# Kernel tuning notes

Hardware: AMD Instinct MI355X
Metric: run time of the kernel (lower is better)

Reference implementation:

```python
import jax, jax.numpy as jnp
import numpy as np
from jax import lax

T, N, E = 12, 10000, 160000
C_IN, C_H, C_OUT = 32, 64, 32
EPS = 1e-5


def _glorot(key, shape):
    fan_in, fan_out = shape[-2] if len(shape) > 1 else shape[0], shape[-1]
    s = (6.0 / (fan_in + fan_out)) ** 0.5
    return jax.random.uniform(key, shape, jnp.float32, -s, s)


def setup_inputs() -> dict:
    key = jax.random.key(0)
    ks = jax.random.split(key, 16)
    inp = {
        "x": jax.random.normal(ks[0], (T, N, C_IN), jnp.float32),
        "edge_index": jax.random.randint(ks[1], (2, E), 0, N, jnp.int32),
        "edge_weight": jax.random.uniform(ks[2], (E,), jnp.float32),
        # layer 1 (input layer): in=C_IN -> C_H
        "conv_w1": _glorot(ks[3], (C_H, C_IN, 3)) * 0.1,
        "conv_b1": jnp.zeros((C_H,), jnp.float32),
        "gamma1": jnp.ones((C_H,), jnp.float32),
        "beta1": jnp.zeros((C_H,), jnp.float32),
        "gcn_w1": _glorot(ks[4], (C_H, C_H)),
        "gcn_b1": jnp.zeros((C_H,), jnp.float32),
        # layer 2 (hidden layer): C_H -> C_H
        "conv_w2": _glorot(ks[5], (C_H, C_H, 3)) * 0.1,
        "conv_b2": jnp.zeros((C_H,), jnp.float32),
        "gamma2": jnp.ones((C_H,), jnp.float32),
        "beta2": jnp.zeros((C_H,), jnp.float32),
        "gcn_w2": _glorot(ks[6], (C_H, C_H)),
        "gcn_b2": jnp.zeros((C_H,), jnp.float32),
        # output linear: C_H -> C_OUT
        "out_w": _glorot(ks[7], (C_H, C_OUT)),
        "out_b": jnp.zeros((C_OUT,), jnp.float32),
    }
    return inp


def _stgcn_layer(x, edge_index, edge_weight, cw, cb, gamma, beta, gw, gb):
    # x: [T, N, C_in]  ->  torch.stack(x).permute(1,2,0) = [N, C_in, T]
    xs = jnp.transpose(x, (1, 2, 0))
    h = lax.conv_general_dilated(xs, cw, (1,), [(1, 1)],
                                 dimension_numbers=("NCH", "OIH", "NCH"))
    h = h + cb[None, :, None]
    # InstanceNorm1d(affine) over the temporal dim
    mu = h.mean(-1, keepdims=True)
    var = ((h - mu) ** 2).mean(-1, keepdims=True)
    h = (h - mu) * lax.rsqrt(var + EPS) * gamma[None, :, None] + beta[None, :, None]
    h = jax.nn.relu(h)
    h = jnp.transpose(h, (2, 0, 1))  # [T, N, C_out]
    # GCNConv per timestep (vectorized over T)
    src, dst = edge_index[0], edge_index[1]
    n = h.shape[1]
    deg = jnp.zeros((n,), h.dtype).at[dst].add(edge_weight) + 1.0  # self-loop weight 1
    dis = lax.rsqrt(deg)
    norm = dis[src] * edge_weight * dis[dst]  # [E]
    xw = jnp.einsum("tnc,cd->tnd", h, gw)  # [T, N, C_out]
    msg = xw[:, src, :] * norm[None, :, None]  # [T, E, C_out]
    agg = jax.vmap(lambda m: jax.ops.segment_sum(m, dst, num_segments=n))(msg)
    agg = agg + (dis * dis)[None, :, None] * xw + gb  # self loop + bias
    return agg


def reference(x, edge_index, edge_weight,
              conv_w1, conv_b1, gamma1, beta1, gcn_w1, gcn_b1,
              conv_w2, conv_b2, gamma2, beta2, gcn_w2, gcn_b2,
              out_w, out_b):
    h = _stgcn_layer(x, edge_index, edge_weight,
                     conv_w1, conv_b1, gamma1, beta1, gcn_w1, gcn_b1)
    h = _stgcn_layer(h, edge_index, edge_weight,
                     conv_w2, conv_b2, gamma2, beta2, gcn_w2, gcn_b2)
    out = jnp.einsum("tnc,co->tno", h, out_w) + out_b  # per-t linear
    return out.mean(axis=0)  # [N, C_OUT]
```

## Files before the change

kernel.cpp:

```cpp
#include <hip/hip_runtime.h>
#include <hip/hip_bf16.h>
#include <stdint.h>

#define MAXDEG 64

typedef short s16x8 __attribute__((ext_vector_type(8)));
typedef short s16x4 __attribute__((ext_vector_type(4)));
typedef float f32x4 __attribute__((ext_vector_type(4)));

static __device__ __forceinline__ float us2f(unsigned short u) {
    union { float f; unsigned int i; } cv; cv.i = ((unsigned int)u) << 16; return cv.f;
}
static __device__ __forceinline__ unsigned short f2us(float f) {
    __hip_bfloat16 h = __float2bfloat16(f);
    return *(unsigned short*)&h;
}

#define WIMG_TOTAL 30720

__global__ void k_build_ell(const int* __restrict__ ei, const float* __restrict__ ew,
                            float* __restrict__ deg, unsigned* __restrict__ cnt,
                            int2* __restrict__ ell, int E)
{
    int e = blockIdx.x * 256 + threadIdx.x;
    if (e >= E) return;
    int s = ei[e], d = ei[E + e];
    float w = ew[e];
    atomicAdd(&deg[d], w);
    unsigned slot = atomicAdd(&cnt[d], 1u);
    if (slot < MAXDEG) ell[(size_t)d * MAXDEG + slot] = make_int2(s, __float_as_int(w));
}

__global__ void k_norm(int2* __restrict__ ell, const unsigned* __restrict__ cnt,
                       const float* __restrict__ deg, int N)
{
    int idx = blockIdx.x * 256 + threadIdx.x;
    if (idx >= N * MAXDEG) return;
    int n = idx >> 6;
    int s = idx & (MAXDEG - 1);
    unsigned dg = cnt[n]; if (dg > MAXDEG) dg = MAXDEG;
    if ((unsigned)s >= dg) return;
    int2 p = ell[idx];
    unsigned sx = (unsigned)p.x;
    float nrm = (sx < (unsigned)N)
        ? rsqrtf(deg[sx] + 1.0f) * __int_as_float(p.y) * rsqrtf(deg[n] + 1.0f) : 0.f;
    ell[idx] = make_int2(p.x, __float_as_int(nrm));
}

__global__ void k_prep(const float* __restrict__ cw1, const float* __restrict__ gw1,
                       const float* __restrict__ cw2, const float* __restrict__ gw2,
                       unsigned short* __restrict__ wimg)
{
    int idx = blockIdx.x * 256 + threadIdx.x;
    if (idx >= WIMG_TOTAL) return;
    float v = 0.f;
    if (idx < 7680) {
        int kk = idx / 2560, r = idx - kk * 2560, cc = r / 40, ci = r - cc * 40;
        if (ci < 32) v = cw1[(cc * 32 + ci) * 3 + kk];
    } else if (idx < 12288) {
        int j = idx - 7680, d = j / 72, cc = j - d * 72;
        if (cc < 64) v = gw1[cc * 64 + d];
    } else if (idx < 26112) {
        int j = idx - 12288;
        int kk = j / 4608, r = j - kk * 4608, cc = r / 72, ci = r - cc * 72;
        if (ci < 64) v = cw2[(cc * 64 + ci) * 3 + kk];
    } else {
        int j = idx - 26112, d = j / 72, cc = j - d * 72;
        if (cc < 64) v = gw2[cc * 64 + d];
    }
    wimg[idx] = f2us(v);
}

#define ACCE(NRM, V0, V1, V2)                                                          \
    a[0] = fmaf(NRM, us2f(V0.x), a[0]);  a[1] = fmaf(NRM, us2f(V0.y), a[1]);           \
    a[2] = fmaf(NRM, us2f(V0.z), a[2]);  a[3] = fmaf(NRM, us2f(V0.w), a[3]);           \
    a[4] = fmaf(NRM, us2f(V1.x), a[4]);  a[5] = fmaf(NRM, us2f(V1.y), a[5]);           \
    a[6] = fmaf(NRM, us2f(V1.z), a[6]);  a[7] = fmaf(NRM, us2f(V1.w), a[7]);           \
    a[8] = fmaf(NRM, us2f(V2.x), a[8]);  a[9] = fmaf(NRM, us2f(V2.y), a[9]);           \
    a[10] = fmaf(NRM, us2f(V2.z), a[10]); a[11] = fmaf(NRM, us2f(V2.w), a[11]);

template<int CIN>
__global__ __launch_bounds__(1024, 4) void k_layer_a(
    const float* __restrict__ x_in,
    const unsigned short* __restrict__ wimg,
    const float* __restrict__ gm, const float* __restrict__ bt,
    unsigned short* __restrict__ xw_out, int N)
{
    constexpr int KT   = CIN / 32;
    constexpr int WSTR = (CIN == 64) ? 72 : 40;
    __shared__ __align__(16) short WT[3 * 64 * WSTR];
    __shared__ __align__(16) short gwT[64 * 72];
    __shared__ __align__(16) short xh[16][14 * 72];

    const int tid = threadIdx.x;
    const int nn = tid >> 6;
    const int c = tid & 63;
    const int m = c & 15;
    const int q = c >> 4;
    const int mrow = (m < 12) ? m : 11;
    int n = blockIdx.x * 16 + nn;
    if (n >= N) n = N - 1;

    {
        const uint4* wt1  = (const uint4*)(wimg);
        const uint4* gwt1 = (const uint4*)(wimg + 7680);
        if (tid < 960) ((uint4*)WT)[tid]  = wt1[tid];
        if (tid < 576) ((uint4*)gwT)[tid] = gwt1[tid];
    }
    #pragma unroll
    for (int it = 0; it < (12 * CIN) / 128; ++it) {
        int i2 = it * 128 + c * 2;
        int t = i2 / CIN, ci = i2 - t * CIN;
        float2 xv = *(const float2*)&x_in[((size_t)t * N + n) * CIN + ci];
        xh[nn][(t + 1) * 72 + ci]     = (short)f2us(xv.x);
        xh[nn][(t + 1) * 72 + ci + 1] = (short)f2us(xv.y);
    }
    if (c < CIN) { xh[nn][c] = 0; xh[nn][13 * 72 + c] = 0; }
    __syncthreads();

    f32x4 acc[4];
    #pragma unroll
    for (int nt = 0; nt < 4; ++nt) acc[nt] = (f32x4){0.f, 0.f, 0.f, 0.f};
    #pragma unroll
    for (int kk = 0; kk < 3; ++kk) {
        #pragma unroll
        for (int kt = 0; kt < KT; ++kt) {
            s16x8 aA = *(const s16x8*)&xh[nn][(mrow + kk) * 72 + kt * 32 + q * 8];
            #pragma unroll
            for (int nt = 0; nt < 4; ++nt) {
                s16x8 bB = *(const s16x8*)&WT[kk * (64 * WSTR) + (nt * 16 + m) * WSTR + kt * 32 + q * 8];
                acc[nt] = __builtin_amdgcn_mfma_f32_16x16x32_bf16(aA, bB, acc[nt], 0, 0, 0);
            }
        }
    }

    #pragma unroll
    for (int nt = 0; nt < 4; ++nt) {
        float s  = acc[nt][0] + acc[nt][1] + acc[nt][2] + acc[nt][3];
        float s2 = acc[nt][0] * acc[nt][0] + acc[nt][1] * acc[nt][1]
                 + acc[nt][2] * acc[nt][2] + acc[nt][3] * acc[nt][3];
        if (q == 3) { s = 0.f; s2 = 0.f; }
        s  += __shfl_xor(s, 16);  s  += __shfl_xor(s, 32);
        s2 += __shfl_xor(s2, 16); s2 += __shfl_xor(s2, 32);
        const float mu  = s * (1.f / 12.f);
        const float var = s2 * (1.f / 12.f) - mu * mu;
        const float scn = rsqrtf(var + 1e-5f) * gm[nt * 16 + m];
        const float sbn = bt[nt * 16 + m];
        if (q < 3) {
            #pragma unroll
            for (int reg = 0; reg < 4; ++reg) {
                float hv = fmaf(acc[nt][reg] - mu, scn, sbn);
                hv = hv > 0.f ? hv : 0.f;
                xh[nn][(q * 4 + reg) * 72 + nt * 16 + m] = (short)f2us(hv);
            }
        }
    }

    s16x8 a2[2];
    #pragma unroll
    for (int kt2 = 0; kt2 < 2; ++kt2)
        a2[kt2] = *(const s16x8*)&xh[nn][mrow * 72 + kt2 * 32 + q * 8];
    f32x4 acc2[4];
    #pragma unroll
    for (int nt = 0; nt < 4; ++nt) acc2[nt] = (f32x4){0.f, 0.f, 0.f, 0.f};
    #pragma unroll
    for (int nt = 0; nt < 4; ++nt) {
        #pragma unroll
        for (int kt2 = 0; kt2 < 2; ++kt2) {
            s16x8 b2 = *(const s16x8*)&gwT[(nt * 16 + m) * 72 + kt2 * 32 + q * 8];
            acc2[nt] = __builtin_amdgcn_mfma_f32_16x16x32_bf16(a2[kt2], b2, acc2[nt], 0, 0, 0);
        }
    }

    unsigned short* dst = xw_out + (size_t)n * 768;
    if (q < 3) {
        #pragma unroll
        for (int nt = 0; nt < 4; ++nt)
            #pragma unroll
            for (int reg = 0; reg < 4; ++reg)
                dst[(q * 4 + reg) * 64 + nt * 16 + m] = f2us(acc2[nt][reg]);
    }
}

__global__ __launch_bounds__(512, 4) void k_gather_a(
    const unsigned short* __restrict__ xw_in,
    const int2* __restrict__ ell, const unsigned* __restrict__ cnt,
    const float* __restrict__ deg, const float* __restrict__ gb,
    const unsigned short* __restrict__ wimg,
    const float* __restrict__ gm, const float* __restrict__ bt,
    unsigned short* __restrict__ rowmean, int N)
{
    constexpr int WSTR = 72;
    __shared__ __align__(16) short WT[3 * 64 * WSTR];
    __shared__ __align__(16) short gwT[64 * 72];
    __shared__ __align__(16) short xh[8][14 * 72];

    const int tid = threadIdx.x;
    const int nn = tid >> 6;
    const int L = tid & 63;
    const int m = L & 15;
    const int q = L >> 4;
    const int mrow = (m < 12) ? m : 11;
    int n = blockIdx.x * 8 + nn;
    if (n >= N) n = N - 1;

    const int2* row = ell + (size_t)n * MAXDEG;
    int2 pl = row[L];
    unsigned dg = cnt[n]; if (dg > MAXDEG) dg = MAXDEG;
    const float dn = rsqrtf(deg[n] + 1.0f);
    const float d2 = dn * dn;
    const unsigned short* self = xw_in + (size_t)n * 768 + L * 4;
    ushort4 v0 = *(const ushort4*)self;
    ushort4 v1 = *(const ushort4*)(self + 256);
    ushort4 v2 = *(const ushort4*)(self + 512);

    {
        const uint4* wt2  = (const uint4*)(wimg + 12288);
        const uint4* gwt2 = (const uint4*)(wimg + 26112);
        for (int g = tid; g < 1728; g += 512) ((uint4*)WT)[g]  = wt2[g];
        for (int g = tid; g < 576;  g += 512) ((uint4*)gwT)[g] = gwt2[g];
    }
    xh[nn][L] = 0; xh[nn][13 * 72 + L] = 0;
    __syncthreads();

    float a[12];
    {
        const int c0 = (L * 4) & 63;
        const float g0 = gb[c0], g1 = gb[c0 + 1], g2 = gb[c0 + 2], g3 = gb[c0 + 3];
        a[0] = fmaf(d2, us2f(v0.x), g0); a[1] = fmaf(d2, us2f(v0.y), g1);
        a[2] = fmaf(d2, us2f(v0.z), g2); a[3] = fmaf(d2, us2f(v0.w), g3);
        a[4] = fmaf(d2, us2f(v1.x), g0); a[5] = fmaf(d2, us2f(v1.y), g1);
        a[6] = fmaf(d2, us2f(v1.z), g2); a[7] = fmaf(d2, us2f(v1.w), g3);
        a[8] = fmaf(d2, us2f(v2.x), g0); a[9] = fmaf(d2, us2f(v2.y), g1);
        a[10] = fmaf(d2, us2f(v2.z), g2); a[11] = fmaf(d2, us2f(v2.w), g3);
    }

    unsigned e = 0;
    for (; e + 8 <= dg; e += 8) {
        ushort4 B0[8], B1[8], B2[8];
        float NR[8];
        #pragma unroll
        for (int i = 0; i < 8; ++i) {
            unsigned sx = (unsigned)__builtin_amdgcn_readlane(pl.x, (int)(e + i));
            NR[i] = __int_as_float(__builtin_amdgcn_readlane(pl.y, (int)(e + i)));
            if (sx >= (unsigned)N) sx = 0;
            const unsigned short* qp = xw_in + (size_t)sx * 768 + L * 4;
            B0[i] = *(const ushort4*)qp;
            B1[i] = *(const ushort4*)(qp + 256);
            B2[i] = *(const ushort4*)(qp + 512);
        }
        #pragma unroll
        for (int i = 0; i < 8; ++i) { ACCE(NR[i], B0[i], B1[i], B2[i]) }
    }
    if (e + 4 <= dg) {
        ushort4 B0[4], B1[4], B2[4];
        float NR[4];
        #pragma unroll
        for (int i = 0; i < 4; ++i) {
            unsigned sx = (unsigned)__builtin_amdgcn_readlane(pl.x, (int)(e + i));
            NR[i] = __int_as_float(__builtin_amdgcn_readlane(pl.y, (int)(e + i)));
            if (sx >= (unsigned)N) sx = 0;
            const unsigned short* qp = xw_in + (size_t)sx * 768 + L * 4;
            B0[i] = *(const ushort4*)qp;
            B1[i] = *(const ushort4*)(qp + 256);
            B2[i] = *(const ushort4*)(qp + 512);
        }
        #pragma unroll
        for (int i = 0; i < 4; ++i) { ACCE(NR[i], B0[i], B1[i], B2[i]) }
        e += 4;
    }
    for (; e < dg; ++e) {
        unsigned sx = (unsigned)__builtin_amdgcn_readlane(pl.x, (int)e);
        float nr = __int_as_float(__builtin_amdgcn_readlane(pl.y, (int)e));
        if (sx >= (unsigned)N) sx = 0;
        const unsigned short* qp = xw_in + (size_t)sx * 768 + L * 4;
        ushort4 w0 = *(const ushort4*)qp;
        ushort4 w1 = *(const ushort4*)(qp + 256);
        ushort4 w2 = *(const ushort4*)(qp + 512);
        ACCE(nr, w0, w1, w2)
    }

    #pragma unroll
    for (int j = 0; j < 3; ++j) {
        s16x4 s4 = { (short)f2us(a[j * 4 + 0]), (short)f2us(a[j * 4 + 1]),
                     (short)f2us(a[j * 4 + 2]), (short)f2us(a[j * 4 + 3]) };
        *(s16x4*)&xh[nn][(j * 4 + q + 1) * 72 + ((L * 4) & 63)] = s4;
    }

    f32x4 acc[4];
    #pragma unroll
    for (int nt = 0; nt < 4; ++nt) acc[nt] = (f32x4){0.f, 0.f, 0.f, 0.f};
    #pragma unroll
    for (int kk = 0; kk < 3; ++kk) {
        #pragma unroll
        for (int kt = 0; kt < 2; ++kt) {
            s16x8 aA = *(const s16x8*)&xh[nn][(mrow + kk) * 72 + kt * 32 + q * 8];
            #pragma unroll
            for (int nt = 0; nt < 4; ++nt) {
                s16x8 bB = *(const s16x8*)&WT[kk * (64 * WSTR) + (nt * 16 + m) * WSTR + kt * 32 + q * 8];
                acc[nt] = __builtin_amdgcn_mfma_f32_16x16x32_bf16(aA, bB, acc[nt], 0, 0, 0);
            }
        }
    }

    #pragma unroll
    for (int nt = 0; nt < 4; ++nt) {
        float s  = acc[nt][0] + acc[nt][1] + acc[nt][2] + acc[nt][3];
        float s2 = acc[nt][0] * acc[nt][0] + acc[nt][1] * acc[nt][1]
                 + acc[nt][2] * acc[nt][2] + acc[nt][3] * acc[nt][3];
        if (q == 3) { s = 0.f; s2 = 0.f; }
        s  += __shfl_xor(s, 16);  s  += __shfl_xor(s, 32);
        s2 += __shfl_xor(s2, 16); s2 += __shfl_xor(s2, 32);
        const float mu  = s * (1.f / 12.f);
        const float var = s2 * (1.f / 12.f) - mu * mu;
        const float scn = rsqrtf(var + 1e-5f) * gm[nt * 16 + m];
        const float sbn = bt[nt * 16 + m];
        if (q < 3) {
            #pragma unroll
            for (int reg = 0; reg < 4; ++reg) {
                float hv = fmaf(acc[nt][reg] - mu, scn, sbn);
                hv = hv > 0.f ? hv : 0.f;
                xh[nn][(q * 4 + reg) * 72 + nt * 16 + m] = (short)f2us(hv);
            }
        }
    }

    s16x8 a2[2];
    #pragma unroll
    for (int kt2 = 0; kt2 < 2; ++kt2)
        a2[kt2] = *(const s16x8*)&xh[nn][mrow * 72 + kt2 * 32 + q * 8];
    f32x4 acc2[4];
    #pragma unroll
    for (int nt = 0; nt < 4; ++nt) acc2[nt] = (f32x4){0.f, 0.f, 0.f, 0.f};
    #pragma unroll
    for (int nt = 0; nt < 4; ++nt) {
        #pragma unroll
        for (int kt2 = 0; kt2 < 2; ++kt2) {
            s16x8 b2 = *(const s16x8*)&gwT[(nt * 16 + m) * 72 + kt2 * 32 + q * 8];
            acc2[nt] = __builtin_amdgcn_mfma_f32_16x16x32_bf16(a2[kt2], b2, acc2[nt], 0, 0, 0);
        }
    }

    #pragma unroll
    for (int nt = 0; nt < 4; ++nt) {
        float pm = (q < 3) ? (acc2[nt][0] + acc2[nt][1] + acc2[nt][2] + acc2[nt][3]) : 0.f;
        pm += __shfl_xor(pm, 16); pm += __shfl_xor(pm, 32);
        if (q == 0)
            rowmean[(size_t)n * 64 + nt * 16 + m] = f2us(pm * (1.f / 12.f));
    }
}

#define FIN_E(EIDX)                                                                    \
    {                                                                                  \
        unsigned sx = (unsigned)__builtin_amdgcn_readlane(pl.x, (int)(EIDX));          \
        float nrm = __int_as_float(__builtin_amdgcn_readlane(pl.y, (int)(EIDX)));      \
        if (sx >= (unsigned)N) sx = 0;                                                 \
        a = fmaf(nrm, us2f(rowmean[(size_t)sx * 64 + L]), a);                          \
    }

__global__ __launch_bounds__(256) void k_final(
    const unsigned short* __restrict__ rowmean, const int2* __restrict__ ell,
    const unsigned* __restrict__ cnt, const float* __restrict__ deg,
    const float* __restrict__ gb,
    const float* __restrict__ ow, const float* __restrict__ ob,
    float* __restrict__ dout, int N)
{
    __shared__ __align__(16) float hbuf[4][64];
    const int tid = threadIdx.x;
    const int nn = tid >> 6, L = tid & 63;
    int n = blockIdx.x * 4 + nn;
    if (n >= N) n = N - 1;
    const float dn = rsqrtf(deg[n] + 1.0f);
    const float d2 = dn * dn;

    const int2* row = ell + (size_t)n * MAXDEG;
    int2 pl = row[L];
    unsigned dg = cnt[n]; if (dg > MAXDEG) dg = MAXDEG;

    float a = fmaf(d2, us2f(rowmean[(size_t)n * 64 + L]), gb[L]);

    unsigned e = 0;
    for (; e + 7 < dg; e += 8) {
        FIN_E(e)     FIN_E(e + 1) FIN_E(e + 2) FIN_E(e + 3)
        FIN_E(e + 4) FIN_E(e + 5) FIN_E(e + 6) FIN_E(e + 7)
    }
    for (; e < dg; ++e) { FIN_E(e) }

    hbuf[nn][L] = a;
    __syncthreads();
    if (L < 32) {
        float oa = ob[L];
        #pragma unroll
        for (int cc = 0; cc < 64; ++cc)
            oa = fmaf(hbuf[nn][cc], ow[cc * 32 + L], oa);
        dout[(size_t)n * 32 + L] = oa;
    }
}

extern "C" void kernel_launch(void* const* d_in, const int* in_sizes, int n_in,
                              void* d_out, int out_size, void* d_ws, size_t ws_size,
                              hipStream_t stream)
{
    const float* x   = (const float*)d_in[0];
    const int*   ei  = (const int*)d_in[1];
    const float* ew  = (const float*)d_in[2];
    const float* cw1 = (const float*)d_in[3];
    const float* gm1 = (const float*)d_in[5];
    const float* bt1 = (const float*)d_in[6];
    const float* gw1 = (const float*)d_in[7];
    const float* gb1 = (const float*)d_in[8];
    const float* cw2 = (const float*)d_in[9];
    const float* gm2 = (const float*)d_in[11];
    const float* bt2 = (const float*)d_in[12];
    const float* gw2 = (const float*)d_in[13];
    const float* gb2 = (const float*)d_in[14];
    const float* ow  = (const float*)d_in[15];
    const float* ob  = (const float*)d_in[16];

    const int N = in_sizes[0] / (12 * 32);
    const int E = in_sizes[2];

    char* p0 = (char*)d_ws;
    char* p = p0;
    float* deg = (float*)p;          p += (size_t)N * 4;
    unsigned* cnt = (unsigned*)p;    p += (size_t)N * 4;
    p = (char*)(((uintptr_t)p + 255) & ~(uintptr_t)255);
    int2* ell = (int2*)p;            p += (size_t)N * MAXDEG * 8;
    p = (char*)(((uintptr_t)p + 255) & ~(uintptr_t)255);
    unsigned short* wimg = (unsigned short*)p; p += (size_t)WIMG_TOTAL * 2;
    p = (char*)(((uintptr_t)p + 255) & ~(uintptr_t)255);
    unsigned short* bufXW1 = (unsigned short*)p; p += (size_t)N * 768 * 2;
    unsigned short* rowmean = (unsigned short*)p; p += (size_t)N * 64 * 2;

    const size_t need = (size_t)(p - p0);
    if (ws_size < need) {
        hipMemsetAsync(d_out, 0, (size_t)out_size * 4, stream);
        return;
    }

    hipMemsetAsync(deg, 0, (size_t)N * 8, stream);

    const int eb   = (E + 255) / 256;
    const int nb16 = (N + 15) / 16;
    const int nb8  = (N + 7) / 8;
    const int nb4  = (N + 3) / 4;
    k_prep<<<(WIMG_TOTAL + 255) / 256, 256, 0, stream>>>(cw1, gw1, cw2, gw2, wimg);
    k_build_ell<<<eb, 256, 0, stream>>>(ei, ew, deg, cnt, ell, E);
    k_norm<<<(N * MAXDEG + 255) / 256, 256, 0, stream>>>(ell, cnt, deg, N);

    k_layer_a<32><<<nb16, 1024, 0, stream>>>(x, wimg, gm1, bt1, bufXW1, N);
    k_gather_a<<<nb8, 512, 0, stream>>>(bufXW1, ell, cnt, deg, gb1,
                                        wimg, gm2, bt2, rowmean, N);
    k_final<<<nb4, 256, 0, stream>>>(rowmean, ell, cnt, deg, gb2, ow, ob, (float*)d_out, N);
}
```

Baseline: 177.9 us.

## Fuse ELL build into layer-1 kernel, compute edge norm on the fly, widen gathers

The separate ELL-build and normalization kernels are removed. Edge insertion now runs in extra blocks appended to the layer-1 conv/GCN launch, and the per-edge normalization is recomputed inside the gather and final kernels from deg[src]. Gathers of the bf16 XW rows use one 16-byte load plus one 8-byte load per neighbor instead of three 8-byte loads, with the channel mapping and the shared-memory writes changed to match. This saves two launches and a pass over the ELL array, at the cost of an extra deg[] lookup and rsqrt per edge and mixing atomic-heavy blocks with MFMA blocks in one grid.

After: 169.6 us. 1.05x faster.

```diff
diff --git a/kernel.cpp b/kernel.cpp
--- a/kernel.cpp
+++ b/kernel.cpp
@@ -17,35 +17,6 @@
 }
 
 #define WIMG_TOTAL 30720
-
-__global__ void k_build_ell(const int* __restrict__ ei, const float* __restrict__ ew,
-                            float* __restrict__ deg, unsigned* __restrict__ cnt,
-                            int2* __restrict__ ell, int E)
-{
-    int e = blockIdx.x * 256 + threadIdx.x;
-    if (e >= E) return;
-    int s = ei[e], d = ei[E + e];
-    float w = ew[e];
-    atomicAdd(&deg[d], w);
-    unsigned slot = atomicAdd(&cnt[d], 1u);
-    if (slot < MAXDEG) ell[(size_t)d * MAXDEG + slot] = make_int2(s, __float_as_int(w));
-}
-
-__global__ void k_norm(int2* __restrict__ ell, const unsigned* __restrict__ cnt,
-                       const float* __restrict__ deg, int N)
-{
-    int idx = blockIdx.x * 256 + threadIdx.x;
-    if (idx >= N * MAXDEG) return;
-    int n = idx >> 6;
-    int s = idx & (MAXDEG - 1);
-    unsigned dg = cnt[n]; if (dg > MAXDEG) dg = MAXDEG;
-    if ((unsigned)s >= dg) return;
-    int2 p = ell[idx];
-    unsigned sx = (unsigned)p.x;
-    float nrm = (sx < (unsigned)N)
-        ? rsqrtf(deg[sx] + 1.0f) * __int_as_float(p.y) * rsqrtf(deg[n] + 1.0f) : 0.f;
-    ell[idx] = make_int2(p.x, __float_as_int(nrm));
-}
 
 __global__ void k_prep(const float* __restrict__ cw1, const float* __restrict__ gw1,
                        const float* __restrict__ cw2, const float* __restrict__ gw2,
@@ -71,21 +42,39 @@
     wimg[idx] = f2us(v);
 }
 
-#define ACCE(NRM, V0, V1, V2)                                                          \
-    a[0] = fmaf(NRM, us2f(V0.x), a[0]);  a[1] = fmaf(NRM, us2f(V0.y), a[1]);           \
-    a[2] = fmaf(NRM, us2f(V0.z), a[2]);  a[3] = fmaf(NRM, us2f(V0.w), a[3]);           \
-    a[4] = fmaf(NRM, us2f(V1.x), a[4]);  a[5] = fmaf(NRM, us2f(V1.y), a[5]);           \
-    a[6] = fmaf(NRM, us2f(V1.z), a[6]);  a[7] = fmaf(NRM, us2f(V1.w), a[7]);           \
-    a[8] = fmaf(NRM, us2f(V2.x), a[8]);  a[9] = fmaf(NRM, us2f(V2.y), a[9]);           \
-    a[10] = fmaf(NRM, us2f(V2.z), a[10]); a[11] = fmaf(NRM, us2f(V2.w), a[11]);
+#define BLO(u) __uint_as_float((unsigned)(u) << 16)
+#define BHI(u) __uint_as_float((unsigned)(u) & 0xffff0000u)
+
+#define ACC2(NRM, WA, WB)                                                              \
+    a[0] = fmaf(NRM, BLO(WA.x), a[0]);   a[1] = fmaf(NRM, BHI(WA.x), a[1]);            \
+    a[2] = fmaf(NRM, BLO(WA.y), a[2]);   a[3] = fmaf(NRM, BHI(WA.y), a[3]);            \
+    a[4] = fmaf(NRM, BLO(WA.z), a[4]);   a[5] = fmaf(NRM, BHI(WA.z), a[5]);            \
+    a[6] = fmaf(NRM, BLO(WA.w), a[6]);   a[7] = fmaf(NRM, BHI(WA.w), a[7]);            \
+    a[8] = fmaf(NRM, us2f(WB.x), a[8]);  a[9] = fmaf(NRM, us2f(WB.y), a[9]);           \
+    a[10] = fmaf(NRM, us2f(WB.z), a[10]); a[11] = fmaf(NRM, us2f(WB.w), a[11]);
 
 template<int CIN>
-__global__ __launch_bounds__(1024, 4) void k_layer_a(
+__global__ __launch_bounds__(1024, 4) void k_layer_build(
     const float* __restrict__ x_in,
     const unsigned short* __restrict__ wimg,
     const float* __restrict__ gm, const float* __restrict__ bt,
-    unsigned short* __restrict__ xw_out, int N)
+    unsigned short* __restrict__ xw_out, int N, int NB,
+    const int* __restrict__ ei, const float* __restrict__ ew,
+    float* __restrict__ deg, unsigned* __restrict__ cnt,
+    int2* __restrict__ ell, int E)
 {
+    if ((int)blockIdx.x >= NB) {
+        int e = ((int)blockIdx.x - NB) * 1024 + (int)threadIdx.x;
+        if (e < E) {
+            int s = ei[e], d = ei[E + e];
+            float w = ew[e];
+            atomicAdd(&deg[d], w);
+            unsigned slot = atomicAdd(&cnt[d], 1u);
+            if (slot < MAXDEG) ell[(size_t)d * MAXDEG + slot] = make_int2(s, __float_as_int(w));
+        }
+        return;
+    }
+
     constexpr int KT   = CIN / 32;
     constexpr int WSTR = (CIN == 64) ? 72 : 40;
     __shared__ __align__(16) short WT[3 * 64 * WSTR];
@@ -209,10 +198,9 @@
     unsigned dg = cnt[n]; if (dg > MAXDEG) dg = MAXDEG;
     const float dn = rsqrtf(deg[n] + 1.0f);
     const float d2 = dn * dn;
-    const unsigned short* self = xw_in + (size_t)n * 768 + L * 4;
-    ushort4 v0 = *(const ushort4*)self;
-    ushort4 v1 = *(const ushort4*)(self + 256);
-    ushort4 v2 = *(const ushort4*)(self + 512);
+    const unsigned short* sp = xw_in + (size_t)n * 768;
+    uint4   sA = *(const uint4*)(sp + 8 * L);
+    ushort4 sB = *(const ushort4*)(sp + 512 + 4 * L);
 
     {
         const uint4* wt2  = (const uint4*)(wimg + 12288);
@@ -225,66 +213,68 @@
 
     float a[12];
     {
-        const int c0 = (L * 4) & 63;
-        const float g0 = gb[c0], g1 = gb[c0 + 1], g2 = gb[c0 + 2], g3 = gb[c0 + 3];
-        a[0] = fmaf(d2, us2f(v0.x), g0); a[1] = fmaf(d2, us2f(v0.y), g1);
-        a[2] = fmaf(d2, us2f(v0.z), g2); a[3] = fmaf(d2, us2f(v0.w), g3);
-        a[4] = fmaf(d2, us2f(v1.x), g0); a[5] = fmaf(d2, us2f(v1.y), g1);
-        a[6] = fmaf(d2, us2f(v1.z), g2); a[7] = fmaf(d2, us2f(v1.w), g3);
-        a[8] = fmaf(d2, us2f(v2.x), g0); a[9] = fmaf(d2, us2f(v2.y), g1);
-        a[10] = fmaf(d2, us2f(v2.z), g2); a[11] = fmaf(d2, us2f(v2.w), g3);
+        const int cb1 = 8 * (L & 7);
+        const int cb2 = (4 * L) & 63;
+        a[0] = fmaf(d2, BLO(sA.x), gb[cb1 + 0]); a[1] = fmaf(d2, BHI(sA.x), gb[cb1 + 1]);
+        a[2] = fmaf(d2, BLO(sA.y), gb[cb1 + 2]); a[3] = fmaf(d2, BHI(sA.y), gb[cb1 + 3]);
+        a[4] = fmaf(d2, BLO(sA.z), gb[cb1 + 4]); a[5] = fmaf(d2, BHI(sA.z), gb[cb1 + 5]);
+        a[6] = fmaf(d2, BLO(sA.w), gb[cb1 + 6]); a[7] = fmaf(d2, BHI(sA.w), gb[cb1 + 7]);
+        a[8] = fmaf(d2, us2f(sB.x), gb[cb2 + 0]); a[9]  = fmaf(d2, us2f(sB.y), gb[cb2 + 1]);
+        a[10] = fmaf(d2, us2f(sB.z), gb[cb2 + 2]); a[11] = fmaf(d2, us2f(sB.w), gb[cb2 + 3]);
     }
 
     unsigned e = 0;
     for (; e + 8 <= dg; e += 8) {
-        ushort4 B0[8], B1[8], B2[8];
-        float NR[8];
+        uint4 A[8]; ushort4 Bv[8]; float NR[8];
         #pragma unroll
         for (int i = 0; i < 8; ++i) {
-            unsigned sx = (unsigned)__builtin_amdgcn_readlane(pl.x, (int)(e + i));
-            NR[i] = __int_as_float(__builtin_amdgcn_readlane(pl.y, (int)(e + i)));
-            if (sx >= (unsigned)N) sx = 0;
-            const unsigned short* qp = xw_in + (size_t)sx * 768 + L * 4;
-            B0[i] = *(const ushort4*)qp;
-            B1[i] = *(const ushort4*)(qp + 256);
-            B2[i] = *(const ushort4*)(qp + 512);
-        }
-        #pragma unroll
-        for (int i = 0; i < 8; ++i) { ACCE(NR[i], B0[i], B1[i], B2[i]) }
+            unsigned sxr = (unsigned)__builtin_amdgcn_readlane(pl.x, (int)(e + i));
+            float w = __int_as_float(__builtin_amdgcn_readlane(pl.y, (int)(e + i)));
+            unsigned sx = (sxr < (unsigned)N) ? sxr : 0u;
+            float nr = rsqrtf(deg[sx] + 1.0f) * w * dn;
+            NR[i] = (sxr < (unsigned)N) ? nr : 0.f;
+            const unsigned short* qp = xw_in + (size_t)sx * 768;
+            A[i]  = *(const uint4*)(qp + 8 * L);
+            Bv[i] = *(const ushort4*)(qp + 512 + 4 * L);
+        }
+        #pragma unroll
+        for (int i = 0; i < 8; ++i) { ACC2(NR[i], A[i], Bv[i]) }
     }
     if (e + 4 <= dg) {
-        ushort4 B0[4], B1[4], B2[4];
-        float NR[4];
+        uint4 A[4]; ushort4 Bv[4]; float NR[4];
         #pragma unroll
         for (int i = 0; i < 4; ++i) {
-            unsigned sx = (unsigned)__builtin_amdgcn_readlane(pl.x, (int)(e + i));
-            NR[i] = __int_as_float(__builtin_amdgcn_readlane(pl.y, (int)(e + i)));
-            if (sx >= (unsigned)N) sx = 0;
-            const unsigned short* qp = xw_in + (size_t)sx * 768 + L * 4;
-            B0[i] = *(const ushort4*)qp;
-            B1[i] = *(const ushort4*)(qp + 256);
-            B2[i] = *(const ushort4*)(qp + 512);
-        }
-        #pragma unroll
-        for (int i = 0; i < 4; ++i) { ACCE(NR[i], B0[i], B1[i], B2[i]) }
+            unsigned sxr = (unsigned)__builtin_amdgcn_readlane(pl.x, (int)(e + i));
+            float w = __int_as_float(__builtin_amdgcn_readlane(pl.y, (int)(e + i)));
+            unsigned sx = (sxr < (unsigned)N) ? sxr : 0u;
+            float nr = rsqrtf(deg[sx] + 1.0f) * w * dn;
+            NR[i] = (sxr < (unsigned)N) ? nr : 0.f;
+            const unsigned short* qp = xw_in + (size_t)sx * 768;
+            A[i]  = *(const uint4*)(qp + 8 * L);
+            Bv[i] = *(const ushort4*)(qp + 512 + 4 * L);
+        }
+        #pragma unroll
+        for (int i = 0; i < 4; ++i) { ACC2(NR[i], A[i], Bv[i]) }
         e += 4;
     }
     for (; e < dg; ++e) {
-        unsigned sx = (unsigned)__builtin_amdgcn_readlane(pl.x, (int)e);
-        float nr = __int_as_float(__builtin_amdgcn_readlane(pl.y, (int)e));
-        if (sx >= (unsigned)N) sx = 0;
-        const unsigned short* qp = xw_in + (size_t)sx * 768 + L * 4;
-        ushort4 w0 = *(const ushort4*)qp;
-        ushort4 w1 = *(const ushort4*)(qp + 256);
-        ushort4 w2 = *(const ushort4*)(qp + 512);
-        ACCE(nr, w0, w1, w2)
-    }
-
-    #pragma unroll
-    for (int j = 0; j < 3; ++j) {
-        s16x4 s4 = { (short)f2us(a[j * 4 + 0]), (short)f2us(a[j * 4 + 1]),
-                     (short)f2us(a[j * 4 + 2]), (short)f2us(a[j * 4 + 3]) };
-        *(s16x4*)&xh[nn][(j * 4 + q + 1) * 72 + ((L * 4) & 63)] = s4;
+        unsigned sxr = (unsigned)__builtin_amdgcn_readlane(pl.x, (int)e);
+        float w = __int_as_float(__builtin_amdgcn_readlane(pl.y, (int)e));
+        unsigned sx = (sxr < (unsigned)N) ? sxr : 0u;
+        float nr = rsqrtf(deg[sx] + 1.0f) * w * dn;
+        if (sxr >= (unsigned)N) nr = 0.f;
+        const unsigned short* qp = xw_in + (size_t)sx * 768;
+        uint4 A = *(const uint4*)(qp + 8 * L);
+        ushort4 Bv = *(const ushort4*)(qp + 512 + 4 * L);
+        ACC2(nr, A, Bv)
+    }
+
+    {
+        s16x8 p1 = { (short)f2us(a[0]), (short)f2us(a[1]), (short)f2us(a[2]), (short)f2us(a[3]),
+                     (short)f2us(a[4]), (short)f2us(a[5]), (short)f2us(a[6]), (short)f2us(a[7]) };
+        *(s16x8*)&xh[nn][((L >> 3) + 1) * 72 + 8 * (L & 7)] = p1;
+        s16x4 p2 = { (short)f2us(a[8]), (short)f2us(a[9]), (short)f2us(a[10]), (short)f2us(a[11]) };
+        *(s16x4*)&xh[nn][((L >> 4) + 9) * 72 + ((4 * L) & 63)] = p2;
     }
 
     f32x4 acc[4];
@@ -352,10 +342,12 @@
 
 #define FIN_E(EIDX)                                                                    \
     {                                                                                  \
-        unsigned sx = (unsigned)__builtin_amdgcn_readlane(pl.x, (int)(EIDX));          \
-        float nrm = __int_as_float(__builtin_amdgcn_readlane(pl.y, (int)(EIDX)));      \
-        if (sx >= (unsigned)N) sx = 0;                                                 \
-        a = fmaf(nrm, us2f(rowmean[(size_t)sx * 64 + L]), a);                          \
+        unsigned sxr = (unsigned)__builtin_amdgcn_readlane(pl.x, (int)(EIDX));         \
+        float w = __int_as_float(__builtin_amdgcn_readlane(pl.y, (int)(EIDX)));        \
+        unsigned sx = (sxr < (unsigned)N) ? sxr : 0u;                                  \
+        float nr = rsqrtf(deg[sx] + 1.0f) * w * dn;                                    \
+        if (sxr >= (unsigned)N) nr = 0.f;                                              \
+        a = fmaf(nr, us2f(rowmean[(size_t)sx * 64 + L]), a);                           \
     }
 
 __global__ __launch_bounds__(256) void k_final(
@@ -440,15 +432,14 @@
 
     hipMemsetAsync(deg, 0, (size_t)N * 8, stream);
 
-    const int eb   = (E + 255) / 256;
     const int nb16 = (N + 15) / 16;
+    const int ebb  = (E + 1023) / 1024;
     const int nb8  = (N + 7) / 8;
     const int nb4  = (N + 3) / 4;
     k_prep<<<(WIMG_TOTAL + 255) / 256, 256, 0, stream>>>(cw1, gw1, cw2, gw2, wimg);
-    k_build_ell<<<eb, 256, 0, stream>>>(ei, ew, deg, cnt, ell, E);
-    k_norm<<<(N * MAXDEG + 255) / 256, 256, 0, stream>>>(ell, cnt, deg, N);
-
-    k_layer_a<32><<<nb16, 1024, 0, stream>>>(x, wimg, gm1, bt1, bufXW1, N);
+
+    k_layer_build<32><<<nb16 + ebb, 1024, 0, stream>>>(x, wimg, gm1, bt1, bufXW1, N, nb16,
+                                                       ei, ew, deg, cnt, ell, E);
     k_gather_a<<<nb8, 512, 0, stream>>>(bufXW1, ell, cnt, deg, gb1,
                                         wimg, gm2, bt2, rowmean, N);
     k_final<<<nb4, 256, 0, stream>>>(rowmean, ell, cnt, deg, gb2, ow, ob, (float*)d_out, N);
```
